# Optimization experiments

Hardware: AMD Instinct MI355X
Metric: run time of the kernel (lower is better)

Reference implementation:

```python
import jax, jax.numpy as jnp
import numpy as np

B, C_IN, C_OUT = 2, 32, 32
N_IN = 128 * 128            # input grid points
N_OUT = 128 * 128           # output grid points
KERNEL_SIZE = 9             # (3-1)*4 + 1 for kernel_shape=[3,4], piecewise_linear basis
NNZ = 1_500_000             # sparse entries in psi (kernel_size, n_out, n_in)


def setup_inputs() -> dict:
    key = jax.random.key(0)
    ks = jax.random.split(key, 8)
    scale = (1.0 / C_IN) ** 0.5  # sqrt(1/groupsize), groups=1
    return {
        "x": jax.random.normal(ks[0], (B, C_IN, N_IN), jnp.float32),
        "quadrature_weights": jax.random.uniform(ks[1], (N_IN,), jnp.float32, 0.5, 1.5) / N_IN,
        "psi_vals": jax.random.uniform(ks[2], (NNZ,), jnp.float32),
        "weight": scale * jax.random.normal(ks[3], (C_OUT, C_IN, KERNEL_SIZE), jnp.float32),
        "bias": jnp.zeros((C_OUT,), jnp.float32),
        "psi_idx_k": jax.random.randint(ks[4], (NNZ,), 0, KERNEL_SIZE, dtype=jnp.int32),
        "psi_idx_out": jax.random.randint(ks[5], (NNZ,), 0, N_OUT, dtype=jnp.int32),
        "psi_idx_in": jax.random.randint(ks[6], (NNZ,), 0, N_IN, dtype=jnp.int32),
        "n_out": N_OUT,
    }


def reference(x, quadrature_weights, psi_vals, weight, bias,
              psi_idx_k, psi_idx_out, psi_idx_in, n_out):
    # x: (B, C, n_in); weight: (O, C, K); psi is sparse (K, n_out, n_in)
    Bb, C, n_in = x.shape
    K = weight.shape[2]
    # pre-multiply by quadrature weights, layout (n_in, B, C) for gather
    xq = (x * quadrature_weights[None, None, :]).transpose(2, 0, 1)
    # gather-weight: contribution of each sparse entry  -> (nnz, B, C)
    contrib = xq[psi_idx_in] * psi_vals[:, None, None]
    # scatter-add into (kernel, out) bins == sparse psi @ xq
    seg = psi_idx_k * n_out + psi_idx_out
    xk = jax.ops.segment_sum(contrib, seg, num_segments=K * n_out)
    xk = xk.reshape(K, n_out, Bb, C)  # (K, n_out, B, C)
    # channel/kernel mixing with learned weight (groups=1)
    out = jnp.einsum("knbc,ock->bon", xk, weight) + bias[None, :, None]
    return out  # (B, out_channels, n_out)
```

## Files before the change

### kernel.cpp

```cpp
#include <hip/hip_runtime.h>

#define N_IN   16384
#define N_OUT  16384
#define KSZ    9
#define CIN    32
#define COUT   32
#define BC     64
#define ROWS   144
#define XSTR   68
#define CHA    4096
#define ECAP_A 32768
#define ECAP_B 2048

__global__ void k_xq(const float* __restrict__ x, const float* __restrict__ qw,
                     float* __restrict__ xq, const float* __restrict__ w,
                     float* __restrict__ wT, int* __restrict__ gcntA,
                     int* __restrict__ gcntB) {
    const int tid = threadIdx.x;
    if (blockIdx.x == 256) {
        for (int i = tid; i < COUT * CIN * KSZ; i += 256) {
            int o = i / (CIN * KSZ);
            int r = i - o * (CIN * KSZ);
            int c = r / KSZ;
            int k = r - c * KSZ;
            wT[((k * 8 + (o >> 2)) * 32 + c) * 4 + (o & 3)] = w[i];
        }
        for (int i = tid; i < 1024; i += 256) gcntB[i] = 0;
        if (tid < 64) gcntA[tid] = 0;
        return;
    }
    __shared__ float tile[64 * 65];
    const int in0 = blockIdx.x * 64;
#pragma unroll
    for (int i = 0; i < 16; ++i) {
        int idx = tid + i * 256;
        int bcl = idx >> 6, inl = idx & 63;
        tile[bcl * 65 + inl] = x[bcl * N_IN + in0 + inl];
    }
    __syncthreads();
#pragma unroll
    for (int i = 0; i < 16; ++i) {
        int idx = tid + i * 256;
        int inl = idx >> 6, bcl = idx & 63;
        xq[(size_t)(in0 + inl) * BC + bcl] = tile[bcl * 65 + inl] * qw[in0 + inl];
    }
}

__global__ __launch_bounds__(512) void k_binA(const float* __restrict__ vals,
        const int* __restrict__ ik, const int* __restrict__ io, const int* __restrict__ ii,
        int* __restrict__ gcntA, float2* __restrict__ sivA, int nnz) {
    __shared__ int    cntE[64];
    __shared__ int    gbase[64];
    __shared__ int    cursor[64];
    __shared__ int    cnt[64];
    __shared__ float2 slist[CHA];
    const int t = threadIdx.x, c = blockIdx.x;
    if (t < 64) cnt[t] = 0;
    __syncthreads();
    const int base = c * CHA;
    const int e0   = base + t * 8;

    float vv[8]; int pk[8]; int bk[8]; bool hv[8];
    if (e0 + 8 <= nnz) {
        int4 a0 = *(const int4*)(io + e0),  a1 = *(const int4*)(io + e0 + 4);
        int4 b0 = *(const int4*)(ii + e0),  b1 = *(const int4*)(ii + e0 + 4);
        int4 k0 = *(const int4*)(ik + e0),  k1 = *(const int4*)(ik + e0 + 4);
        float4 d0 = *(const float4*)(vals + e0), d1 = *(const float4*)(vals + e0 + 4);
        int ov[8] = {a0.x, a0.y, a0.z, a0.w, a1.x, a1.y, a1.z, a1.w};
        int iv[8] = {b0.x, b0.y, b0.z, b0.w, b1.x, b1.y, b1.z, b1.w};
        int kv[8] = {k0.x, k0.y, k0.z, k0.w, k1.x, k1.y, k1.z, k1.w};
        float dv[8] = {d0.x, d0.y, d0.z, d0.w, d1.x, d1.y, d1.z, d1.w};
#pragma unroll
        for (int j = 0; j < 8; ++j) {
            hv[j] = true;
            bk[j] = ov[j] >> 8;
            pk[j] = ((ov[j] >> 4) << 22) | (iv[j] << 8) | (kv[j] * 16 + (ov[j] & 15));
            vv[j] = dv[j];
        }
    } else {
#pragma unroll
        for (int j = 0; j < 8; ++j) {
            int e = e0 + j;
            hv[j] = (e < nnz);
            if (hv[j]) {
                int o = io[e];
                bk[j] = o >> 8;
                pk[j] = ((o >> 4) << 22) | (ii[e] << 8) | (ik[e] * 16 + (o & 15));
                vv[j] = vals[e];
            } else { bk[j] = 0; pk[j] = 0; vv[j] = 0.f; }
        }
    }
#pragma unroll
    for (int j = 0; j < 8; ++j) if (hv[j]) atomicAdd(&cnt[bk[j]], 1);
    __syncthreads();
    if (t < 64) {
        int cv = cnt[t];
        gbase[t] = t * ECAP_A + (cv ? atomicAdd(&gcntA[t], cv) : 0);
        int v = cv;
#pragma unroll
        for (int off = 1; off < 64; off <<= 1) {
            int u = __shfl_up(v, off);
            if (t >= off) v += u;
        }
        cntE[t]   = v - cv;
        cursor[t] = v - cv;
    }
    __syncthreads();
#pragma unroll
    for (int j = 0; j < 8; ++j) {
        if (hv[j]) {
            int pos = atomicAdd(&cursor[bk[j]], 1);
            slist[pos] = make_float2(vv[j], __int_as_float(pk[j]));
        }
    }
    __syncthreads();
    const int m = min(nnz - base, CHA);
    for (int p = t; p < m; p += 512) {
        float2 f = slist[p];
        int cb = (int)((unsigned)__float_as_int(f.y) >> 26);
        int dest = gbase[cb] + (p - cntE[cb]);
        if (dest < (cb + 1) * ECAP_A) sivA[dest] = f;
    }
}

__global__ __launch_bounds__(512) void k_binB(const float2* __restrict__ sivA,
        const int* __restrict__ gcntA, int* __restrict__ gcntB,
        float2* __restrict__ sivB) {
    __shared__ float2 slist[2048];
    __shared__ int cnt16[16], gb16[16], cur16[16];
    const int t  = threadIdx.x;
    const int cb = blockIdx.x >> 2;
    const int q  = blockIdx.x & 3;
    const int mA = min(gcntA[cb], ECAP_A);
    const int q0 = (mA * q) >> 2;
    const int q1 = (mA * (q + 1)) >> 2;
    const float2* src = sivA + (size_t)cb * ECAP_A;

    for (int start = q0; start < q1; start += 2048) {
        const int cm = min(2048, q1 - start);
        if (t < 16) cnt16[t] = 0;
        __syncthreads();
        float2 ent[4]; bool hv[4];
#pragma unroll
        for (int j = 0; j < 4; ++j) {
            int i = start + t + j * 512;
            hv[j] = (i < start + cm);
            if (hv[j]) {
                ent[j] = src[i];
                atomicAdd(&cnt16[((unsigned)__float_as_int(ent[j].y) >> 22) & 15], 1);
            }
        }
        __syncthreads();
        if (t < 16) {
            int cv = cnt16[t];
            int fg = (cb << 4) + t;
            gb16[t] = fg * ECAP_B + (cv ? atomicAdd(&gcntB[fg], cv) : 0);
            int v = cv;
#pragma unroll
            for (int off = 1; off < 16; off <<= 1) {
                int u = __shfl_up(v, off);
                if (t >= off) v += u;
            }
            cnt16[t] = v - cv;
            cur16[t] = v - cv;
        }
        __syncthreads();
#pragma unroll
        for (int j = 0; j < 4; ++j) {
            if (hv[j]) {
                int pos = atomicAdd(&cur16[((unsigned)__float_as_int(ent[j].y) >> 22) & 15], 1);
                slist[pos] = ent[j];
            }
        }
        __syncthreads();
        for (int p = t; p < cm; p += 512) {
            float2 f = slist[p];
            unsigned fg = (unsigned)__float_as_int(f.y) >> 22;
            int fl = fg & 15;
            int dest = gb16[fl] + (p - cnt16[fl]);
            if (dest < (int)((fg + 1) * ECAP_B)) sivB[dest] = f;
        }
        __syncthreads();
    }
}

__global__ __launch_bounds__(512) void k_fused5(const float* __restrict__ xq,
        const float2* __restrict__ sivB, const int* __restrict__ gcntB,
        const float* __restrict__ wT, const float* __restrict__ bias,
        float* __restrict__ out) {
    __shared__ float  sxk[80 * XSTR];
    __shared__ float2 slist[ECAP_B];
    __shared__ int    rowStart[ROWS + 1];
    __shared__ int    cursor[ROWS];
    const int tid  = threadIdx.x;
    const int lane = tid & 63;
    const int wv   = __builtin_amdgcn_readfirstlane(tid >> 6);
    const int bkt  = blockIdx.x;

    if (tid < ROWS) rowStart[tid] = 0;
    __syncthreads();

    const int m = min(gcntB[bkt], ECAP_B);
    const float2* src = sivB + (size_t)bkt * ECAP_B;
    float2 ent[4]; bool have[4];
#pragma unroll
    for (int j = 0; j < 4; ++j) {
        int i = tid + j * 512;
        have[j] = (i < m);
        if (have[j]) {
            ent[j] = src[i];
            atomicAdd(&rowStart[__float_as_int(ent[j].y) & 0xFF], 1);
        }
    }
    __syncthreads();
    if (wv == 0) {
        int carry = 0;
#pragma unroll
        for (int i0 = 0; i0 < 192; i0 += 64) {
            int idx = i0 + lane;
            int v = (idx < ROWS) ? rowStart[idx] : 0;
            int orig = v;
#pragma unroll
            for (int off = 1; off < 64; off <<= 1) {
                int u = __shfl_up(v, off);
                if (lane >= off) v += u;
            }
            if (idx < ROWS) {
                int excl = carry + v - orig;
                rowStart[idx] = excl;
                cursor[idx]   = excl;
            }
            carry += __shfl(v, 63);
        }
        if (lane == 0) rowStart[ROWS] = m;
    }
    __syncthreads();
#pragma unroll
    for (int j = 0; j < 4; ++j) {
        if (have[j]) {
            int pos = atomicAdd(&cursor[__float_as_int(ent[j].y) & 0xFF], 1);
            slist[pos] = ent[j];
        }
    }

    const char* xqb   = (const char*)xq;
    const int   lane4 = lane * 4;
    const int   h     = lane >> 4;
    const int   nl    = lane & 15;
    float acc[4] = {0.f, 0.f, 0.f, 0.f};

#pragma unroll
    for (int ph = 0; ph < 2; ++ph) {
        const int rbase = ph ? 80 : 0;
        const int rend  = ph ? 144 : 80;
        const int nrows = rend - rbase;
        for (int i = tid; i < nrows * XSTR; i += 512) sxk[i] = 0.f;
        __syncthreads();
        for (int r = rbase + wv; r < rend; r += 8) {
            const int a = rowStart[r], b = rowStart[r + 1];
            if (a >= b) continue;
            float acc0 = 0.f, acc1 = 0.f, acc2 = 0.f, acc3 = 0.f;
            int i = a;
            for (; i + 7 < b; i += 8) {
                float2 v0 = slist[i],     v1 = slist[i + 1], v2 = slist[i + 2], v3 = slist[i + 3];
                float2 v4 = slist[i + 4], v5 = slist[i + 5], v6 = slist[i + 6], v7 = slist[i + 7];
                acc0 += *(const float*)(xqb + ((__float_as_int(v0.y) & 0x3FFF00) + lane4)) * v0.x;
                acc1 += *(const float*)(xqb + ((__float_as_int(v1.y) & 0x3FFF00) + lane4)) * v1.x;
                acc2 += *(const float*)(xqb + ((__float_as_int(v2.y) & 0x3FFF00) + lane4)) * v2.x;
                acc3 += *(const float*)(xqb + ((__float_as_int(v3.y) & 0x3FFF00) + lane4)) * v3.x;
                acc0 += *(const float*)(xqb + ((__float_as_int(v4.y) & 0x3FFF00) + lane4)) * v4.x;
                acc1 += *(const float*)(xqb + ((__float_as_int(v5.y) & 0x3FFF00) + lane4)) * v5.x;
                acc2 += *(const float*)(xqb + ((__float_as_int(v6.y) & 0x3FFF00) + lane4)) * v6.x;
                acc3 += *(const float*)(xqb + ((__float_as_int(v7.y) & 0x3FFF00) + lane4)) * v7.x;
            }
            for (; i + 3 < b; i += 4) {
                float2 v0 = slist[i], v1 = slist[i + 1], v2 = slist[i + 2], v3 = slist[i + 3];
                acc0 += *(const float*)(xqb + ((__float_as_int(v0.y) & 0x3FFF00) + lane4)) * v0.x;
                acc1 += *(const float*)(xqb + ((__float_as_int(v1.y) & 0x3FFF00) + lane4)) * v1.x;
                acc2 += *(const float*)(xqb + ((__float_as_int(v2.y) & 0x3FFF00) + lane4)) * v2.x;
                acc3 += *(const float*)(xqb + ((__float_as_int(v3.y) & 0x3FFF00) + lane4)) * v3.x;
            }
            for (; i < b; ++i) {
                float2 v = slist[i];
                acc0 += *(const float*)(xqb + ((__float_as_int(v.y) & 0x3FFF00) + lane4)) * v.x;
            }
            sxk[(r - rbase) * XSTR + lane] = (acc0 + acc1) + (acc2 + acc3);
        }
        __syncthreads();
        if (lane < 32) {
            const int kbase = ph ? 5 : 0;
            const int kcnt  = ph ? 4 : 5;
            for (int kk = 0; kk < kcnt; ++kk) {
                const float* xr = &sxk[(kk * 16 + nl) * XSTR + h * 32];
                const float* wp = &wT[((kbase + kk) * 8 + wv) * 128];
#pragma unroll
                for (int c4 = 0; c4 < 8; ++c4) {
                    float4 xv = *(const float4*)&xr[c4 * 4];
#pragma unroll
                    for (int cc = 0; cc < 4; ++cc) {
                        float xval = (&xv.x)[cc];
#pragma unroll
                        for (int j = 0; j < 4; ++j)
                            acc[j] += xval * wp[(c4 * 4 + cc) * 4 + j];
                    }
                }
            }
        }
        __syncthreads();
    }

    if (lane < 32) {
        const int n0 = bkt * 16;
#pragma unroll
        for (int j = 0; j < 4; ++j) {
            int o = wv * 4 + j;
            out[((size_t)h * COUT + o) * N_OUT + n0 + nl] = acc[j] + bias[o];
        }
    }
}

extern "C" void kernel_launch(void* const* d_in, const int* in_sizes, int n_in,
                              void* d_out, int out_size, void* d_ws, size_t ws_size,
                              hipStream_t stream) {
    const float* x    = (const float*)d_in[0];
    const float* qw   = (const float*)d_in[1];
    const float* vals = (const float*)d_in[2];
    const float* w    = (const float*)d_in[3];
    const float* bias = (const float*)d_in[4];
    const int*   ik   = (const int*)d_in[5];
    const int*   io   = (const int*)d_in[6];
    const int*   ii   = (const int*)d_in[7];
    const int    nnz  = in_sizes[2];
    const int    nchA = (nnz + CHA - 1) / CHA;

    char* ws = (char*)d_ws;
    float*  xq    = (float*)ws;  ws += (size_t)N_IN * BC * 4;
    float2* sivA  = (float2*)ws; ws += (size_t)64 * ECAP_A * 8;
    float2* sivB  = (float2*)ws; ws += (size_t)1024 * ECAP_B * 8;
    int*    gcntA = (int*)ws;    ws += 64 * 4;
    int*    gcntB = (int*)ws;    ws += 1024 * 4;
    float*  wT    = (float*)ws;  ws += (size_t)COUT * CIN * KSZ * 4;

    k_xq    <<<257, 256, 0, stream>>>(x, qw, xq, w, wT, gcntA, gcntB);
    k_binA  <<<nchA, 512, 0, stream>>>(vals, ik, io, ii, gcntA, sivA, nnz);
    k_binB  <<<256, 512, 0, stream>>>(sivA, gcntA, gcntB, sivB);
    k_fused5<<<1024, 512, 0, stream>>>(xq, sivB, gcntB, wT, bias, (float*)d_out);
}
```

Measured before the change: 156.5 us.

## Drop second binning pass; fused kernel filters its bucket from coarser bins

The first binning pass now uses 256 coarse buckets of 64 output points instead of 64 buckets of 256. The second scatter pass (k_binB) and its workspace are removed. Each fused block reads its parent coarse bucket (about 4x the entries it needs) and keeps only the entries for its own 16-point group. This saves one kernel launch and a global write and read round trip, but every block now scans four times as many entries and pays extra shared-memory atomics, reusing the sxk buffer as scratch.

New measurement: 148.9 us. 1.05x faster.

```diff
diff --git a/kernel.cpp b/kernel.cpp
--- a/kernel.cpp
+++ b/kernel.cpp
@@ -6,16 +6,16 @@
 #define CIN    32
 #define COUT   32
 #define BC     64
+#define NCB    256
+#define CHA    4096
+#define ECAP_A 8192
 #define ROWS   144
 #define XSTR   68
-#define CHA    4096
-#define ECAP_A 32768
-#define ECAP_B 2048
+#define SCAP   2048
 
 __global__ void k_xq(const float* __restrict__ x, const float* __restrict__ qw,
                      float* __restrict__ xq, const float* __restrict__ w,
-                     float* __restrict__ wT, int* __restrict__ gcntA,
-                     int* __restrict__ gcntB) {
+                     float* __restrict__ wT, int* __restrict__ gcntA) {
     const int tid = threadIdx.x;
     if (blockIdx.x == 256) {
         for (int i = tid; i < COUT * CIN * KSZ; i += 256) {
@@ -25,8 +25,7 @@
             int k = r - c * KSZ;
             wT[((k * 8 + (o >> 2)) * 32 + c) * 4 + (o & 3)] = w[i];
         }
-        for (int i = tid; i < 1024; i += 256) gcntB[i] = 0;
-        if (tid < 64) gcntA[tid] = 0;
+        if (tid < NCB) gcntA[tid] = 0;
         return;
     }
     __shared__ float tile[64 * 65];
@@ -49,13 +48,10 @@
 __global__ __launch_bounds__(512) void k_binA(const float* __restrict__ vals,
         const int* __restrict__ ik, const int* __restrict__ io, const int* __restrict__ ii,
         int* __restrict__ gcntA, float2* __restrict__ sivA, int nnz) {
-    __shared__ int    cntE[64];
-    __shared__ int    gbase[64];
-    __shared__ int    cursor[64];
-    __shared__ int    cnt[64];
+    __shared__ int    cnt[NCB], cntE[NCB], gbase[NCB], cursor[NCB];
     __shared__ float2 slist[CHA];
     const int t = threadIdx.x, c = blockIdx.x;
-    if (t < 64) cnt[t] = 0;
+    if (t < NCB) cnt[t] = 0;
     __syncthreads();
     const int base = c * CHA;
     const int e0   = base + t * 8;
@@ -73,8 +69,8 @@
 #pragma unroll
         for (int j = 0; j < 8; ++j) {
             hv[j] = true;
-            bk[j] = ov[j] >> 8;
-            pk[j] = ((ov[j] >> 4) << 22) | (iv[j] << 8) | (kv[j] * 16 + (ov[j] & 15));
+            bk[j] = ov[j] >> 6;
+            pk[j] = (int)(((unsigned)(ov[j] >> 4) << 22)) | (iv[j] << 8) | (kv[j] * 16 + (ov[j] & 15));
             vv[j] = dv[j];
         }
     } else {
@@ -84,8 +80,8 @@
             hv[j] = (e < nnz);
             if (hv[j]) {
                 int o = io[e];
-                bk[j] = o >> 8;
-                pk[j] = ((o >> 4) << 22) | (ii[e] << 8) | (ik[e] * 16 + (o & 15));
+                bk[j] = o >> 6;
+                pk[j] = (int)(((unsigned)(o >> 4) << 22)) | (ii[e] << 8) | (ik[e] * 16 + (o & 15));
                 vv[j] = vals[e];
             } else { bk[j] = 0; pk[j] = 0; vv[j] = 0.f; }
         }
@@ -93,17 +89,26 @@
 #pragma unroll
     for (int j = 0; j < 8; ++j) if (hv[j]) atomicAdd(&cnt[bk[j]], 1);
     __syncthreads();
-    if (t < 64) {
+    if (t < NCB) {
         int cv = cnt[t];
         gbase[t] = t * ECAP_A + (cv ? atomicAdd(&gcntA[t], cv) : 0);
-        int v = cv;
-#pragma unroll
-        for (int off = 1; off < 64; off <<= 1) {
-            int u = __shfl_up(v, off);
-            if (t >= off) v += u;
-        }
-        cntE[t]   = v - cv;
-        cursor[t] = v - cv;
+    }
+    if (t < 64) {
+        int carry = 0;
+#pragma unroll
+        for (int seg = 0; seg < 4; ++seg) {
+            int idx = seg * 64 + t;
+            int v = cnt[idx];
+            int orig = v;
+#pragma unroll
+            for (int off = 1; off < 64; off <<= 1) {
+                int u = __shfl_up(v, off);
+                if (t >= off) v += u;
+            }
+            cntE[idx]   = carry + v - orig;
+            cursor[idx] = carry + v - orig;
+            carry += __shfl(v, 63);
+        }
     }
     __syncthreads();
 #pragma unroll
@@ -117,102 +122,47 @@
     const int m = min(nnz - base, CHA);
     for (int p = t; p < m; p += 512) {
         float2 f = slist[p];
-        int cb = (int)((unsigned)__float_as_int(f.y) >> 26);
+        int cb = (int)((unsigned)__float_as_int(f.y) >> 24);
         int dest = gbase[cb] + (p - cntE[cb]);
         if (dest < (cb + 1) * ECAP_A) sivA[dest] = f;
     }
 }
 
-__global__ __launch_bounds__(512) void k_binB(const float2* __restrict__ sivA,
-        const int* __restrict__ gcntA, int* __restrict__ gcntB,
-        float2* __restrict__ sivB) {
-    __shared__ float2 slist[2048];
-    __shared__ int cnt16[16], gb16[16], cur16[16];
-    const int t  = threadIdx.x;
-    const int cb = blockIdx.x >> 2;
-    const int q  = blockIdx.x & 3;
-    const int mA = min(gcntA[cb], ECAP_A);
-    const int q0 = (mA * q) >> 2;
-    const int q1 = (mA * (q + 1)) >> 2;
-    const float2* src = sivA + (size_t)cb * ECAP_A;
-
-    for (int start = q0; start < q1; start += 2048) {
-        const int cm = min(2048, q1 - start);
-        if (t < 16) cnt16[t] = 0;
-        __syncthreads();
-        float2 ent[4]; bool hv[4];
-#pragma unroll
-        for (int j = 0; j < 4; ++j) {
-            int i = start + t + j * 512;
-            hv[j] = (i < start + cm);
-            if (hv[j]) {
-                ent[j] = src[i];
-                atomicAdd(&cnt16[((unsigned)__float_as_int(ent[j].y) >> 22) & 15], 1);
-            }
-        }
-        __syncthreads();
-        if (t < 16) {
-            int cv = cnt16[t];
-            int fg = (cb << 4) + t;
-            gb16[t] = fg * ECAP_B + (cv ? atomicAdd(&gcntB[fg], cv) : 0);
-            int v = cv;
-#pragma unroll
-            for (int off = 1; off < 16; off <<= 1) {
-                int u = __shfl_up(v, off);
-                if (t >= off) v += u;
-            }
-            cnt16[t] = v - cv;
-            cur16[t] = v - cv;
-        }
-        __syncthreads();
-#pragma unroll
-        for (int j = 0; j < 4; ++j) {
-            if (hv[j]) {
-                int pos = atomicAdd(&cur16[((unsigned)__float_as_int(ent[j].y) >> 22) & 15], 1);
-                slist[pos] = ent[j];
-            }
-        }
-        __syncthreads();
-        for (int p = t; p < cm; p += 512) {
-            float2 f = slist[p];
-            unsigned fg = (unsigned)__float_as_int(f.y) >> 22;
-            int fl = fg & 15;
-            int dest = gb16[fl] + (p - cnt16[fl]);
-            if (dest < (int)((fg + 1) * ECAP_B)) sivB[dest] = f;
-        }
-        __syncthreads();
-    }
-}
-
-__global__ __launch_bounds__(512) void k_fused5(const float* __restrict__ xq,
-        const float2* __restrict__ sivB, const int* __restrict__ gcntB,
+__global__ __launch_bounds__(512) void k_fused6(const float* __restrict__ xq,
+        const float2* __restrict__ sivA, const int* __restrict__ gcntA,
         const float* __restrict__ wT, const float* __restrict__ bias,
         float* __restrict__ out) {
-    __shared__ float  sxk[80 * XSTR];
-    __shared__ float2 slist[ECAP_B];
+    __shared__ __align__(16) float sxk[80 * XSTR];
+    __shared__ float2 slist[SCAP];
     __shared__ int    rowStart[ROWS + 1];
     __shared__ int    cursor[ROWS];
+    __shared__ int    mcur;
     const int tid  = threadIdx.x;
     const int lane = tid & 63;
     const int wv   = __builtin_amdgcn_readfirstlane(tid >> 6);
-    const int bkt  = blockIdx.x;
+    const unsigned f = blockIdx.x;
 
     if (tid < ROWS) rowStart[tid] = 0;
-    __syncthreads();
-
-    const int m = min(gcntB[bkt], ECAP_B);
-    const float2* src = sivB + (size_t)bkt * ECAP_B;
-    float2 ent[4]; bool have[4];
-#pragma unroll
-    for (int j = 0; j < 4; ++j) {
-        int i = tid + j * 512;
-        have[j] = (i < m);
-        if (have[j]) {
-            ent[j] = src[i];
-            atomicAdd(&rowStart[__float_as_int(ent[j].y) & 0xFF], 1);
-        }
-    }
-    __syncthreads();
+    if (tid == 0) mcur = 0;
+    __syncthreads();
+
+    const int cb = (int)(f >> 2);
+    const int mA = min(gcntA[cb], ECAP_A);
+    const float2* src = sivA + (size_t)cb * ECAP_A;
+    float2* tmp = (float2*)sxk;
+    for (int i = tid; i < mA; i += 512) {
+        float2 v = src[i];
+        unsigned fid = (unsigned)__float_as_int(v.y) >> 22;
+        if (fid == f) {
+            int pos = atomicAdd(&mcur, 1);
+            if (pos < SCAP) {
+                tmp[pos] = v;
+                atomicAdd(&rowStart[__float_as_int(v.y) & 0xFF], 1);
+            }
+        }
+    }
+    __syncthreads();
+    const int m2 = min(mcur, SCAP);
     if (wv == 0) {
         int carry = 0;
 #pragma unroll
@@ -232,16 +182,15 @@
             }
             carry += __shfl(v, 63);
         }
-        if (lane == 0) rowStart[ROWS] = m;
-    }
-    __syncthreads();
-#pragma unroll
-    for (int j = 0; j < 4; ++j) {
-        if (have[j]) {
-            int pos = atomicAdd(&cursor[__float_as_int(ent[j].y) & 0xFF], 1);
-            slist[pos] = ent[j];
-        }
-    }
+        if (lane == 0) rowStart[ROWS] = carry;
+    }
+    __syncthreads();
+    for (int i = tid; i < m2; i += 512) {
+        float2 v = tmp[i];
+        int pos = atomicAdd(&cursor[__float_as_int(v.y) & 0xFF], 1);
+        slist[pos] = v;
+    }
+    __syncthreads();
 
     const char* xqb   = (const char*)xq;
     const int   lane4 = lane * 4;
@@ -310,7 +259,7 @@
     }
 
     if (lane < 32) {
-        const int n0 = bkt * 16;
+        const int n0 = (int)f * 16;
 #pragma unroll
         for (int j = 0; j < 4; ++j) {
             int o = wv * 4 + j;
@@ -335,14 +284,11 @@
 
     char* ws = (char*)d_ws;
     float*  xq    = (float*)ws;  ws += (size_t)N_IN * BC * 4;
-    float2* sivA  = (float2*)ws; ws += (size_t)64 * ECAP_A * 8;
-    float2* sivB  = (float2*)ws; ws += (size_t)1024 * ECAP_B * 8;
-    int*    gcntA = (int*)ws;    ws += 64 * 4;
-    int*    gcntB = (int*)ws;    ws += 1024 * 4;
+    float2* sivA  = (float2*)ws; ws += (size_t)NCB * ECAP_A * 8;
+    int*    gcntA = (int*)ws;    ws += NCB * 4;
     float*  wT    = (float*)ws;  ws += (size_t)COUT * CIN * KSZ * 4;
 
-    k_xq    <<<257, 256, 0, stream>>>(x, qw, xq, w, wT, gcntA, gcntB);
+    k_xq    <<<257, 256, 0, stream>>>(x, qw, xq, w, wT, gcntA);
     k_binA  <<<nchA, 512, 0, stream>>>(vals, ik, io, ii, gcntA, sivA, nnz);
-    k_binB  <<<256, 512, 0, stream>>>(sivA, gcntA, gcntB, sivB);
-    k_fused5<<<1024, 512, 0, stream>>>(xq, sivB, gcntB, wT, bias, (float*)d_out);
-}
+    k_fused6<<<1024, 512, 0, stream>>>(xq, sivA, gcntA, wT, bias, (float*)d_out);
+}
```
